# Optimization experiments

Hardware: AMD Instinct MI355X
Metric: run time of the kernel (lower is better)

Reference implementation:

```python
import jax, jax.numpy as jnp
import numpy as np

NUM_HEADS = 8
D_MODEL = 512
HEAD_DIM = D_MODEL // NUM_HEADS
LN_EPS = 1e-5


def setup_inputs() -> dict:
    key = jax.random.key(0)
    ks = jax.random.split(key, 12)
    B, S = 8, 1024
    P = 2 * S - 1  # relative position length
    s = 0.02
    return {
        "x": jax.random.normal(ks[0], (B, S, D_MODEL), jnp.float32),
        "pos_emb": jax.random.normal(ks[1], (P, D_MODEL), jnp.float32),
        "ln_w": jnp.ones((D_MODEL,), jnp.float32),
        "ln_b": jnp.zeros((D_MODEL,), jnp.float32),
        "Wq": jax.random.normal(ks[2], (D_MODEL, D_MODEL), jnp.float32) * s,
        "bq": jax.random.normal(ks[3], (D_MODEL,), jnp.float32) * s,
        "Wk": jax.random.normal(ks[4], (D_MODEL, D_MODEL), jnp.float32) * s,
        "bk": jax.random.normal(ks[5], (D_MODEL,), jnp.float32) * s,
        "Wv": jax.random.normal(ks[6], (D_MODEL, D_MODEL), jnp.float32) * s,
        "bv": jax.random.normal(ks[7], (D_MODEL,), jnp.float32) * s,
        "Wo": jax.random.normal(ks[8], (D_MODEL, D_MODEL), jnp.float32) * s,
        "bo": jax.random.normal(ks[9], (D_MODEL,), jnp.float32) * s,
        "Wp": jax.random.normal(ks[10], (D_MODEL, D_MODEL), jnp.float32) * s,
        "pos_bias_u": jax.random.normal(ks[11], (D_MODEL,), jnp.float32) * s,
        "pos_bias_v": jax.random.normal(jax.random.fold_in(key, 99), (D_MODEL,), jnp.float32) * s,
    }


def _rel_shift(x):
    # x: [B, H, S, P] -> Transformer-XL relative shift, return [B, H, S, S]
    b, h, s, p = x.shape
    x = jnp.pad(x, ((0, 0), (0, 0), (0, 0), (1, 0)))  # pad one zero column on left
    x = x.reshape(b, h, p + 1, s)[:, :, 1:, :]
    x = x.reshape(b, h, s, p)
    return x[:, :, :, :s]


def reference(x, pos_emb, ln_w, ln_b, Wq, bq, Wk, bk, Wv, bv, Wo, bo, Wp,
              pos_bias_u, pos_bias_v):
    B, S, D = x.shape
    H, hd = NUM_HEADS, HEAD_DIM
    # LayerNorm
    mu = jnp.mean(x, axis=-1, keepdims=True)
    var = jnp.mean(jnp.square(x - mu), axis=-1, keepdims=True)
    h_ = (x - mu) * jax.lax.rsqrt(var + LN_EPS) * ln_w + ln_b
    # Projections (torch Linear: y = x @ W.T + b)
    q = (h_ @ Wq.T + bq).reshape(B, S, H, hd).transpose(0, 2, 1, 3)  # [B,H,S,hd]
    k = (h_ @ Wk.T + bk).reshape(B, S, H, hd).transpose(0, 2, 1, 3)
    v = (h_ @ Wv.T + bv).reshape(B, S, H, hd).transpose(0, 2, 1, 3)
    bias_u = pos_bias_u.reshape(1, H, 1, hd)
    bias_v = pos_bias_v.reshape(1, H, 1, hd)
    content = jnp.einsum('bhqd,bhkd->bhqk', q + bias_u, k)
    # Positional projection: [P, D] -> [H, P, hd]
    p = (pos_emb @ Wp.T).reshape(-1, H, hd).transpose(1, 0, 2)
    pos_score = jnp.einsum('bhqd,hpd->bhqp', q + bias_v, p)
    pos_score = _rel_shift(pos_score)
    scale = 1.0 / np.sqrt(hd).astype(np.float32)
    attn = jax.nn.softmax((content + pos_score) * scale, axis=-1)
    out = jnp.einsum('bhqk,bhkd->bhqd', attn, v)
    out = out.transpose(0, 2, 1, 3).reshape(B, S, D)
    out = out @ Wo.T + bo
    return x + out
```

## Files before the change

kernel.cpp:

```cpp
#include <hip/hip_runtime.h>
#include <hip/hip_bf16.h>


typedef __attribute__((ext_vector_type(8))) short  s16x8;
typedef __attribute__((ext_vector_type(8))) __bf16 bfv8;
typedef __attribute__((ext_vector_type(4))) float  f32x4;
typedef __attribute__((ext_vector_type(4))) unsigned u32x4;

__device__ __forceinline__ float b2f(short s){
  unsigned u = ((unsigned)(unsigned short)s) << 16;
  float f; __builtin_memcpy(&f, &u, 4); return f;
}
__device__ __forceinline__ short f2b(float f){
  unsigned u; __builtin_memcpy(&u, &f, 4);
  u = (u + 0x7fffu + ((u >> 16) & 1u)) >> 16;
  return (short)u;
}
__device__ __forceinline__ unsigned pk2(float lo, float hi){
  __hip_bfloat162 t = __float22bfloat162_rn(make_float2(lo, hi));
  unsigned u; __builtin_memcpy(&u, &t, 4); return u;
}
__device__ __forceinline__ f32x4 MFMA(s16x8 a, s16x8 b, f32x4 c){
  return __builtin_amdgcn_mfma_f32_16x16x32_bf16(
      __builtin_bit_cast(bfv8, a), __builtin_bit_cast(bfv8, b), c, 0, 0, 0);
}
__device__ __forceinline__ void gload_lds16(const void* g, void* l){
  __builtin_amdgcn_global_load_lds(
      (const __attribute__((address_space(1))) void*)g,
      (__attribute__((address_space(3))) void*)l, 16, 0, 0);
}
__device__ __forceinline__ void cvt8(const float* in, short* out, size_t i8){
  f32x4 a = *(const f32x4*)(in + i8*8);
  f32x4 b = *(const f32x4*)(in + i8*8 + 4);
  u32x4 o;
  o[0] = pk2(a[0],a[1]); o[1] = pk2(a[2],a[3]);
  o[2] = pk2(b[0],b[1]); o[3] = pk2(b[2],b[3]);
  *(u32x4*)(out + i8*8) = o;
}

__global__ __launch_bounds__(256) void prep_kernel(
    const float* __restrict__ Wq, const float* __restrict__ Wk,
    const float* __restrict__ Wv, const float* __restrict__ Wo,
    const float* __restrict__ Wp, const float* __restrict__ pos,
    const float* __restrict__ x, const float* __restrict__ lnw, const float* __restrict__ lnb,
    short* __restrict__ wqkv, short* __restrict__ wo, short* __restrict__ wp,
    short* __restrict__ posbf, short* __restrict__ h_bf)
{
  int bid = blockIdx.x, tid = threadIdx.x;
  if(bid < 640){
    int w = bid >> 7;
    size_t i = (size_t)(bid & 127)*256 + tid;
    const float* src; short* dst;
    if(w == 0){ src = Wq; dst = wqkv; }
    else if(w == 1){ src = Wk; dst = wqkv + 262144; }
    else if(w == 2){ src = Wv; dst = wqkv + 524288; }
    else if(w == 3){ src = Wo; dst = wo; }
    else { src = Wp; dst = wp; }
    cvt8(src, dst, i);
  } else if(bid < 1152){
    size_t i = (size_t)(bid - 640)*256 + tid;
    if(i < 131008) cvt8(pos, posbf, i);
  } else {
    int row = (bid - 1152)*4 + (tid >> 6);
    int lane = tid & 63;
    const float* xr = x + (size_t)row*512;
    f32x4 v0 = *(const f32x4*)(xr + lane*8);
    f32x4 v1 = *(const f32x4*)(xr + lane*8 + 4);
    float s  = v0[0]+v0[1]+v0[2]+v0[3]+v1[0]+v1[1]+v1[2]+v1[3];
    float s2 = v0[0]*v0[0]+v0[1]*v0[1]+v0[2]*v0[2]+v0[3]*v0[3]
             + v1[0]*v1[0]+v1[1]*v1[1]+v1[2]*v1[2]+v1[3]*v1[3];
    #pragma unroll
    for(int m=1;m<64;m<<=1){ s += __shfl_xor(s,m); s2 += __shfl_xor(s2,m); }
    float mu = s * (1.0f/512.0f);
    float rs = rsqrtf(s2*(1.0f/512.0f) - mu*mu + 1e-5f);
    float y[8];
    #pragma unroll
    for(int e=0;e<8;e++){
      float xv = (e<4)? v0[e] : v1[e-4];
      int d = lane*8 + e;
      y[e] = (xv - mu)*rs*lnw[d] + lnb[d];
    }
    u32x4 o;
    o[0]=pk2(y[0],y[1]); o[1]=pk2(y[2],y[3]); o[2]=pk2(y[4],y[5]); o[3]=pk2(y[6],y[7]);
    *(u32x4*)(h_bf + (size_t)row*512 + lane*8) = o;
  }
}

__global__ __launch_bounds__(256) void gemm_fused(
    const short* __restrict__ h_bf, const short* __restrict__ wqkv,
    const float* __restrict__ bq, const float* __restrict__ bk, const float* __restrict__ bv,
    const short* __restrict__ posbf, const short* __restrict__ wp,
    short* __restrict__ q_sw, short* __restrict__ k_sw, short* __restrict__ v_sw,
    short* __restrict__ p_sw)
{
  __shared__ __align__(16) short smem[9216];
  short* At = smem;
  short* Bt = smem + 4096;
  int bid = blockIdx.x, tid = threadIdx.x;
  int wave = tid >> 6, lane = tid & 63;
  int quad = lane >> 4, l16 = lane & 15;
  int srow = lane >> 2, scol = (lane & 3)*8;
  if(bid < 768){
    int bx = bid % 12, by = bid / 12;
    int m0 = by*128, n0 = bx*128;
    int wm = wave >> 1, wn = wave & 1;
    f32x4 acc[4][4] = {};
    for(int k0=0; k0<512; k0+=32){
      #pragma unroll
      for(int c=0;c<2;c++){
        int rb = (wave + 4*c)*16;
        gload_lds16(h_bf + (size_t)(m0 + rb + srow)*512 + k0 + scol, At + rb*32);
        gload_lds16(wqkv + (size_t)(n0 + rb + srow)*512 + k0 + scol, Bt + rb*32);
      }
      __syncthreads();
      s16x8 af[4], bfr[4];
      #pragma unroll
      for(int i=0;i<4;i++) af[i]  = *(const s16x8*)(At + (wm*64 + i*16 + l16)*32 + quad*8);
      #pragma unroll
      for(int j=0;j<4;j++) bfr[j] = *(const s16x8*)(Bt + (wn*64 + j*16 + l16)*32 + quad*8);
      #pragma unroll
      for(int i=0;i<4;i++)
        #pragma unroll
        for(int j=0;j<4;j++)
          acc[i][j] = MFMA(af[i], bfr[j], acc[i][j]);
      __syncthreads();
    }
    int seg = bx >> 2;
    int nseg = (bx & 3)*128;
    int bb = by >> 3;
    const float* bsrc = (seg==0)? bq : (seg==1)? bk : bv;
    float bias_j[4];
    #pragma unroll
    for(int j=0;j<4;j++) bias_j[j] = bsrc[nseg + wn*64 + j*16 + l16];
    if(seg < 2){
      short* dst = seg ? k_sw : q_sw;
      #pragma unroll
      for(int h2=0; h2<2; h2++){
        if(wm == h2){
          #pragma unroll
          for(int i=0;i<4;i++){
            int lr = i*16 + quad*4;
            #pragma unroll
            for(int j=0;j<4;j++){
              int cl = wn*64 + j*16 + l16;
              unsigned p01 = pk2(acc[i][j][0]+bias_j[j], acc[i][j][1]+bias_j[j]);
              unsigned p23 = pk2(acc[i][j][2]+bias_j[j], acc[i][j][3]+bias_j[j]);
              smem[(lr+0)*136 + cl] = (short)p01;
              smem[(lr+1)*136 + cl] = (short)(p01>>16);
              smem[(lr+2)*136 + cl] = (short)p23;
              smem[(lr+3)*136 + cl] = (short)(p23>>16);
            }
          }
        }
        __syncthreads();
        #pragma unroll
        for(int it=0; it<4; it++){
          int ci = it*4 + wave;
          int hs = ci >> 2, tb = ci & 3;
          s16x8 vv = *(const s16x8*)(smem + (tb*16 + l16)*136 + hs*32 + quad*8);
          int hh = (nseg>>6) + (hs>>1);
          int tg = ((m0 + h2*64)>>4) + tb;
          size_t chunk = ((size_t)((bb*8 + hh)*64 + tg))*2 + (hs&1);
          *(s16x8*)(dst + chunk*512 + (size_t)lane*8) = vv;
        }
        __syncthreads();
      }
    } else {
      #pragma unroll
      for(int h2=0; h2<2; h2++){
        int jt = by*2 + h2;
        if(wm == h2){
          #pragma unroll
          for(int i=0;i<4;i++){
            int tl = i*16 + quad*4;
            #pragma unroll
            for(int j=0;j<4;j++){
              int dl = wn*64 + j*16 + l16;
              unsigned p01 = pk2(acc[i][j][0]+bias_j[j], acc[i][j][1]+bias_j[j]);
              unsigned p23 = pk2(acc[i][j][2]+bias_j[j], acc[i][j][3]+bias_j[j]);
              unsigned* w2 = (unsigned*)(smem + dl*72 + tl);
              w2[0] = p01; w2[1] = p23;
            }
          }
        }
        __syncthreads();
        #pragma unroll
        for(int it=0; it<4; it++){
          int ci = it*4 + wave;
          int hl = ci>>3, ds = (ci>>1)&3, jk = ci&1;
          s16x8 vv = *(const s16x8*)(smem + (hl*64 + ds*16 + l16)*72 + jk*32 + quad*8);
          int hh = (nseg>>6) + hl;
          size_t chunk = (((size_t)((bb*8 + hh)*16 + jt))*4 + ds)*2 + jk;
          *(s16x8*)(v_sw + chunk*512 + (size_t)lane*8) = vv;
        }
        __syncthreads();
      }
    }
  } else {
    int pid = bid - 768;
    int bx = pid % 8, by = pid / 8;
    int m0 = by*64, n0 = bx*64;
    int wm = wave >> 1, wn = wave & 1;
    f32x4 acc[2][2] = {};
    for(int k0=0; k0<512; k0+=32){
      int rb = wave*16;
      int ra = m0 + rb + srow; if(ra > 2046) ra = 2046;
      gload_lds16(posbf + (size_t)ra*512 + k0 + scol, At + rb*32);
      gload_lds16(wp + (size_t)(n0 + rb + srow)*512 + k0 + scol, Bt + rb*32);
      __syncthreads();
      s16x8 af[2], bfr[2];
      #pragma unroll
      for(int i=0;i<2;i++) af[i]  = *(const s16x8*)(At + (wm*32 + i*16 + l16)*32 + quad*8);
      #pragma unroll
      for(int j=0;j<2;j++) bfr[j] = *(const s16x8*)(Bt + (wn*32 + j*16 + l16)*32 + quad*8);
      #pragma unroll
      for(int i=0;i<2;i++)
        #pragma unroll
        for(int j=0;j<2;j++)
          acc[i][j] = MFMA(af[i], bfr[j], acc[i][j]);
      __syncthreads();
    }
    #pragma unroll
    for(int i=0;i<2;i++){
      int rowb = m0 + wm*32 + i*16 + quad*4;
      #pragma unroll
      for(int j=0;j<2;j++){
        int col = n0 + wn*32 + j*16 + l16;
        int hh = col>>6, ks = (col>>5)&1, qd = (col>>3)&3, e = col&7;
        int rblk = rowb>>4;
        size_t base = ((size_t)(((hh*128+rblk)*2+ks)*64) + qd*16)*8 + e;
        #pragma unroll
        for(int r=0;r<4;r++)
          p_sw[base + (size_t)(quad*4+r)*8] = f2b(acc[i][j][r]);
      }
    }
  }
}

__global__ __launch_bounds__(256) void attn_kernel(
    const short* __restrict__ q_sw, const short* __restrict__ k_sw,
    const short* __restrict__ v_sw, const short* __restrict__ p_sw,
    const float* __restrict__ bu, const float* __restrict__ bvv,
    short* __restrict__ out)
{
  __shared__ __align__(16) float combf[4160];
  int tid = threadIdx.x;
  int wave = tid >> 6, lane = tid & 63, quad = lane >> 4, l16 = lane & 15;
  int h = blockIdx.y, b = blockIdx.z, bh = b*8 + h;
  int iblk = blockIdx.x;
  int iw = iblk*16;
  short* pw = (short*)combf + wave*1152;

  const short* qb = q_sw + (size_t)bh*65536;
  const short* kb = k_sw + (size_t)bh*65536;
  const short* vb = v_sw + (size_t)bh*65536;
  const short* pb = p_sw + (size_t)h*131072;

  s16x8 qu[2], qv[2];
  #pragma unroll
  for(int ks=0;ks<2;ks++){
    s16x8 qr = *(const s16x8*)(qb + ((size_t)(iblk*2+ks)*64 + lane)*8);
    short tu[8], tv[8];
    #pragma unroll
    for(int e=0;e<8;e++){
      int d = h*64 + ks*32 + quad*8 + e;
      float f = b2f(qr[e]);
      tu[e] = f2b((f + bu[d]) * 0.125f);
      tv[e] = f2b((f + bvv[d]) * 0.125f);
    }
    qu[ks] = *(s16x8*)tu; qv[ks] = *(s16x8*)tv;
  }

  s16x8 ones;
  #pragma unroll
  for(int e=0;e<8;e++) ones[e] = (short)0x3F80;

  int srcl[4]; bool lo[4];
  #pragma unroll
  for(int r=0;r<4;r++){
    int il = quad*4 + r;
    srcl[r] = quad*16 + ((l16 + 15 - il) & 15);
    lo[r]   = (l16 <= il);
  }

  f32x4 oacc[4] = {};
  f32x4 lacc = {};

  #pragma unroll
  for(int t=0; t<4; t++){
    int jt = wave*4 + t;
    int rb0 = (jt*64 - iw + 1008) >> 4;
    f32x4 ps[5];
    #pragma unroll
    for(int nt=0;nt<5;nt++){
      f32x4 a = {};
      #pragma unroll
      for(int ks=0;ks<2;ks++){
        s16x8 pf = *(const s16x8*)(pb + ((size_t)((rb0+nt)*2+ks)*64 + lane)*8);
        a = MFMA(qv[ks], pf, a);
      }
      ps[nt] = a;
    }
    float rot[4][5];
    #pragma unroll
    for(int r=0;r<4;r++)
      #pragma unroll
      for(int nt=0;nt<5;nt++) rot[r][nt] = __shfl(ps[nt][r], srcl[r]);
    float pe[4][4];
    #pragma unroll
    for(int js=0;js<4;js++){
      f32x4 c0;
      #pragma unroll
      for(int r=0;r<4;r++) c0[r] = lo[r] ? rot[r][js] : rot[r][js+1];
      f32x4 a = c0;
      #pragma unroll
      for(int ks=0;ks<2;ks++){
        s16x8 kf = *(const s16x8*)(kb + ((size_t)((jt*4+js)*2+ks)*64 + lane)*8);
        a = MFMA(qu[ks], kf, a);
      }
      #pragma unroll
      for(int r=0;r<4;r++) pe[js][r] = __expf(a[r]);
    }
    #pragma unroll
    for(int js=0;js<4;js++){
      int col = js*16 + l16;
      unsigned p01 = pk2(pe[js][0], pe[js][1]);
      unsigned p23 = pk2(pe[js][2], pe[js][3]);
      pw[(quad*4+0)*72 + col] = (short)p01;
      pw[(quad*4+1)*72 + col] = (short)(p01>>16);
      pw[(quad*4+2)*72 + col] = (short)p23;
      pw[(quad*4+3)*72 + col] = (short)(p23>>16);
    }
    #pragma unroll
    for(int jk=0;jk<2;jk++){
      s16x8 pf = *(const s16x8*)(pw + l16*72 + jk*32 + quad*8);
      #pragma unroll
      for(int ds=0;ds<4;ds++){
        s16x8 vf = *(const s16x8*)(vb + ((size_t)((jt*4+ds)*2+jk)*64 + lane)*8);
        oacc[ds] = MFMA(pf, vf, oacc[ds]);
      }
      lacc = MFMA(pf, ones, lacc);
    }
  }
  __syncthreads();
  float* comb  = combf;
  float* lcomb = combf + 4096;
  #pragma unroll
  for(int e=0;e<16;e++) comb[wave*1024 + e*64 + lane] = oacc[e>>2][e&3];
  if(l16 == 0){
    #pragma unroll
    for(int r=0;r<4;r++) lcomb[wave*16 + quad*4 + r] = lacc[r];
  }
  __syncthreads();
  #pragma unroll
  for(int i=0;i<4;i++){
    int s = i*256 + tid;
    int e = s >> 6, lsrc = s & 63;
    int ds = e >> 2, rr = e & 3;
    int il = (lsrc >> 4)*4 + rr;
    int dim = ds*16 + (lsrc & 15);
    float o = comb[s] + comb[1024+s] + comb[2048+s] + comb[3072+s];
    float l = lcomb[il] + lcomb[16+il] + lcomb[32+il] + lcomb[48+il];
    float rl = __builtin_amdgcn_rcpf(l);
    out[((size_t)(b*1024 + iw + il)*512) + h*64 + dim] = f2b(o * rl);
  }
}

__global__ __launch_bounds__(256) void gemm_out(
    const short* __restrict__ A, const short* __restrict__ B,
    const float* __restrict__ bias, const float* __restrict__ resid,
    float* __restrict__ Cout)
{
  __shared__ __align__(16) short At[64*32];
  __shared__ __align__(16) short Bt[64*32];
  int tid = threadIdx.x;
  int wave = tid >> 6, lane = tid & 63;
  int quad = lane >> 4, l16 = lane & 15;
  int wm = wave >> 1, wn = wave & 1;
  int m0 = blockIdx.y*64, n0 = blockIdx.x*64;
  int srow = lane >> 2, scol = (lane & 3)*8;
  f32x4 acc[2][2] = {};
  for(int k0=0; k0<512; k0+=32){
    int rb = wave*16;
    gload_lds16(A + (size_t)(m0 + rb + srow)*512 + k0 + scol, At + rb*32);
    gload_lds16(B + (size_t)(n0 + rb + srow)*512 + k0 + scol, Bt + rb*32);
    __syncthreads();
    s16x8 af[2], bfr[2];
    #pragma unroll
    for(int i=0;i<2;i++) af[i]  = *(const s16x8*)(At + (wm*32 + i*16 + l16)*32 + quad*8);
    #pragma unroll
    for(int j=0;j<2;j++) bfr[j] = *(const s16x8*)(Bt + (wn*32 + j*16 + l16)*32 + quad*8);
    #pragma unroll
    for(int i=0;i<2;i++)
      #pragma unroll
      for(int j=0;j<2;j++)
        acc[i][j] = MFMA(af[i], bfr[j], acc[i][j]);
    __syncthreads();
  }
  #pragma unroll
  for(int i=0;i<2;i++){
    int rowb = m0 + wm*32 + i*16 + quad*4;
    #pragma unroll
    for(int j=0;j<2;j++){
      int col = n0 + wn*32 + j*16 + l16;
      float bv = bias[col];
      #pragma unroll
      for(int r=0;r<4;r++){
        size_t idx = (size_t)(rowb + r)*512 + col;
        Cout[idx] = acc[i][j][r] + bv + resid[idx];
      }
    }
  }
}

extern "C" void kernel_launch(void* const* d_in, const int* in_sizes, int n_in,
                              void* d_out, int out_size, void* d_ws, size_t ws_size,
                              hipStream_t stream)
{
  const float* x    = (const float*)d_in[0];
  const float* pos  = (const float*)d_in[1];
  const float* lnw  = (const float*)d_in[2];
  const float* lnb  = (const float*)d_in[3];
  const float* Wq   = (const float*)d_in[4];
  const float* bq   = (const float*)d_in[5];
  const float* Wk   = (const float*)d_in[6];
  const float* bk   = (const float*)d_in[7];
  const float* Wv   = (const float*)d_in[8];
  const float* bv   = (const float*)d_in[9];
  const float* Wo   = (const float*)d_in[10];
  const float* bo   = (const float*)d_in[11];
  const float* Wp   = (const float*)d_in[12];
  const float* pbu  = (const float*)d_in[13];
  const float* pbv  = (const float*)d_in[14];
  float* out = (float*)d_out;

  char* ws = (char*)d_ws;
  short* h_bf    = (short*)(ws);
  short* q_sw    = (short*)(ws + ( 8u<<20));
  short* k_sw    = (short*)(ws + (16u<<20));
  short* v_sw    = (short*)(ws + (24u<<20));
  short* a_bf    = (short*)(ws + (32u<<20));
  short* p_sw    = (short*)(ws + (40u<<20));
  short* pos_bf  = (short*)(ws + (42u<<20));
  short* wqkv_bf = (short*)(ws + (44u<<20));
  short* wo_bf   = (short*)(ws + (47u<<20));
  short* wp_bf   = (short*)(ws + (47u<<20) + (512u<<10));

  prep_kernel<<<dim3(3200), 256, 0, stream>>>(Wq, Wk, Wv, Wo, Wp, pos,
                                              x, lnw, lnb,
                                              wqkv_bf, wo_bf, wp_bf, pos_bf, h_bf);
  gemm_fused<<<dim3(1024), 256, 0, stream>>>(h_bf, wqkv_bf, bq, bk, bv,
                                             pos_bf, wp_bf,
                                             q_sw, k_sw, v_sw, p_sw);
  attn_kernel<<<dim3(64,8,8), 256, 0, stream>>>(q_sw, k_sw, v_sw, p_sw, pbu, pbv, a_bf);
  gemm_out<<<dim3(8,128), 256, 0, stream>>>(a_bf, wo_bf, bo, x, out);
  (void)in_sizes; (void)n_in; (void)out_size; (void)ws_size;
}
```

Before: 211.0 us.

## Process two query sub-blocks per attention block to reuse K, V and P fragments

Each attention workgroup now handles 32 query rows (two 16-row sub-blocks) instead of 16, so every K, V and positional fragment loaded from global memory feeds two sets of MFMAs. The positional tiles are shared across the two sub-blocks through a 6-tile sliding window, since the second sub-block's relative-position window is offset by one tile. The grid is halved, shared memory doubled, launch bounds set to 3 blocks per CU, and s_setprio hints wrap the MFMA phases. The cost is more registers per thread and fewer workgroups, which could reduce occupancy and latency hiding.

```diff
diff --git a/kernel.cpp b/kernel.cpp
--- a/kernel.cpp
+++ b/kernel.cpp
@@ -237,38 +237,41 @@
   }
 }
 
-__global__ __launch_bounds__(256) void attn_kernel(
+__global__ __launch_bounds__(256, 3) void attn_kernel(
     const short* __restrict__ q_sw, const short* __restrict__ k_sw,
     const short* __restrict__ v_sw, const short* __restrict__ p_sw,
     const float* __restrict__ bu, const float* __restrict__ bvv,
     short* __restrict__ out)
 {
-  __shared__ __align__(16) float combf[4160];
+  __shared__ __align__(16) float combf[8320];
   int tid = threadIdx.x;
   int wave = tid >> 6, lane = tid & 63, quad = lane >> 4, l16 = lane & 15;
   int h = blockIdx.y, b = blockIdx.z, bh = b*8 + h;
-  int iblk = blockIdx.x;
-  int iw = iblk*16;
-  short* pw = (short*)combf + wave*1152;
+  int qblk = blockIdx.x;
+  int iw = qblk*32;
+  short* pw = (short*)combf + wave*2304;
 
   const short* qb = q_sw + (size_t)bh*65536;
   const short* kb = k_sw + (size_t)bh*65536;
   const short* vb = v_sw + (size_t)bh*65536;
   const short* pb = p_sw + (size_t)h*131072;
 
-  s16x8 qu[2], qv[2];
-  #pragma unroll
-  for(int ks=0;ks<2;ks++){
-    s16x8 qr = *(const s16x8*)(qb + ((size_t)(iblk*2+ks)*64 + lane)*8);
-    short tu[8], tv[8];
-    #pragma unroll
-    for(int e=0;e<8;e++){
-      int d = h*64 + ks*32 + quad*8 + e;
-      float f = b2f(qr[e]);
-      tu[e] = f2b((f + bu[d]) * 0.125f);
-      tv[e] = f2b((f + bvv[d]) * 0.125f);
-    }
-    qu[ks] = *(s16x8*)tu; qv[ks] = *(s16x8*)tv;
+  s16x8 qu[2][2], qv[2][2];
+  #pragma unroll
+  for(int s=0;s<2;s++){
+    #pragma unroll
+    for(int ks=0;ks<2;ks++){
+      s16x8 qr = *(const s16x8*)(qb + ((size_t)((qblk*2+s)*2+ks)*64 + lane)*8);
+      short tu[8], tv[8];
+      #pragma unroll
+      for(int e=0;e<8;e++){
+        int d = h*64 + ks*32 + quad*8 + e;
+        float f = b2f(qr[e]);
+        tu[e] = f2b((f + bu[d]) * 0.125f);
+        tv[e] = f2b((f + bvv[d]) * 0.125f);
+      }
+      qu[s][ks] = *(s16x8*)tu; qv[s][ks] = *(s16x8*)tv;
+    }
   }
 
   s16x8 ones;
@@ -283,86 +286,117 @@
     lo[r]   = (l16 <= il);
   }
 
-  f32x4 oacc[4] = {};
-  f32x4 lacc = {};
+  f32x4 oacc[2][4] = {};
+  f32x4 lacc[2] = {};
 
   #pragma unroll
   for(int t=0; t<4; t++){
     int jt = wave*4 + t;
     int rb0 = (jt*64 - iw + 1008) >> 4;
-    f32x4 ps[5];
-    #pragma unroll
-    for(int nt=0;nt<5;nt++){
-      f32x4 a = {};
-      #pragma unroll
-      for(int ks=0;ks<2;ks++){
-        s16x8 pf = *(const s16x8*)(pb + ((size_t)((rb0+nt)*2+ks)*64 + lane)*8);
-        a = MFMA(qv[ks], pf, a);
-      }
-      ps[nt] = a;
-    }
-    float rot[4][5];
-    #pragma unroll
-    for(int r=0;r<4;r++)
-      #pragma unroll
-      for(int nt=0;nt<5;nt++) rot[r][nt] = __shfl(ps[nt][r], srcl[r]);
-    float pe[4][4];
+    f32x4 ps0[5], ps1[5];
+    __builtin_amdgcn_s_setprio(1);
+    #pragma unroll
+    for(int nt=0;nt<6;nt++){
+      int rbp = rb0 - 1 + nt;
+      s16x8 pf0 = *(const s16x8*)(pb + ((size_t)(rbp*2+0)*64 + lane)*8);
+      s16x8 pf1 = *(const s16x8*)(pb + ((size_t)(rbp*2+1)*64 + lane)*8);
+      if(nt >= 1){
+        f32x4 a = {};
+        a = MFMA(qv[0][0], pf0, a);
+        a = MFMA(qv[0][1], pf1, a);
+        ps0[nt-1] = a;
+      }
+      if(nt <= 4){
+        f32x4 a = {};
+        a = MFMA(qv[1][0], pf0, a);
+        a = MFMA(qv[1][1], pf1, a);
+        ps1[nt] = a;
+      }
+    }
+    __builtin_amdgcn_s_setprio(0);
+    float rot0[4][5], rot1[4][5];
+    #pragma unroll
+    for(int r=0;r<4;r++){
+      #pragma unroll
+      for(int nt=0;nt<5;nt++){
+        rot0[r][nt] = __shfl(ps0[nt][r], srcl[r]);
+        rot1[r][nt] = __shfl(ps1[nt][r], srcl[r]);
+      }
+    }
     #pragma unroll
     for(int js=0;js<4;js++){
-      f32x4 c0;
-      #pragma unroll
-      for(int r=0;r<4;r++) c0[r] = lo[r] ? rot[r][js] : rot[r][js+1];
-      f32x4 a = c0;
-      #pragma unroll
-      for(int ks=0;ks<2;ks++){
-        s16x8 kf = *(const s16x8*)(kb + ((size_t)((jt*4+js)*2+ks)*64 + lane)*8);
-        a = MFMA(qu[ks], kf, a);
-      }
-      #pragma unroll
-      for(int r=0;r<4;r++) pe[js][r] = __expf(a[r]);
-    }
-    #pragma unroll
-    for(int js=0;js<4;js++){
+      s16x8 kf0 = *(const s16x8*)(kb + ((size_t)((jt*4+js)*2+0)*64 + lane)*8);
+      s16x8 kf1 = *(const s16x8*)(kb + ((size_t)((jt*4+js)*2+1)*64 + lane)*8);
       int col = js*16 + l16;
-      unsigned p01 = pk2(pe[js][0], pe[js][1]);
-      unsigned p23 = pk2(pe[js][2], pe[js][3]);
-      pw[(quad*4+0)*72 + col] = (short)p01;
-      pw[(quad*4+1)*72 + col] = (short)(p01>>16);
-      pw[(quad*4+2)*72 + col] = (short)p23;
-      pw[(quad*4+3)*72 + col] = (short)(p23>>16);
-    }
+      {
+        f32x4 c0;
+        #pragma unroll
+        for(int r=0;r<4;r++) c0[r] = lo[r] ? rot0[r][js] : rot0[r][js+1];
+        f32x4 a = MFMA(qu[0][0], kf0, c0);
+        a = MFMA(qu[0][1], kf1, a);
+        unsigned p01 = pk2(__expf(a[0]), __expf(a[1]));
+        unsigned p23 = pk2(__expf(a[2]), __expf(a[3]));
+        pw[(quad*4+0)*72 + col] = (short)p01;
+        pw[(quad*4+1)*72 + col] = (short)(p01>>16);
+        pw[(quad*4+2)*72 + col] = (short)p23;
+        pw[(quad*4+3)*72 + col] = (short)(p23>>16);
+      }
+      {
+        f32x4 c0;
+        #pragma unroll
+        for(int r=0;r<4;r++) c0[r] = lo[r] ? rot1[r][js] : rot1[r][js+1];
+        f32x4 a = MFMA(qu[1][0], kf0, c0);
+        a = MFMA(qu[1][1], kf1, a);
+        unsigned p01 = pk2(__expf(a[0]), __expf(a[1]));
+        unsigned p23 = pk2(__expf(a[2]), __expf(a[3]));
+        pw[1152 + (quad*4+0)*72 + col] = (short)p01;
+        pw[1152 + (quad*4+1)*72 + col] = (short)(p01>>16);
+        pw[1152 + (quad*4+2)*72 + col] = (short)p23;
+        pw[1152 + (quad*4+3)*72 + col] = (short)(p23>>16);
+      }
+    }
+    __builtin_amdgcn_s_setprio(1);
     #pragma unroll
     for(int jk=0;jk<2;jk++){
-      s16x8 pf = *(const s16x8*)(pw + l16*72 + jk*32 + quad*8);
+      s16x8 pa0 = *(const s16x8*)(pw + l16*72 + jk*32 + quad*8);
+      s16x8 pa1 = *(const s16x8*)(pw + 1152 + l16*72 + jk*32 + quad*8);
+      lacc[0] = MFMA(pa0, ones, lacc[0]);
+      lacc[1] = MFMA(pa1, ones, lacc[1]);
       #pragma unroll
       for(int ds=0;ds<4;ds++){
         s16x8 vf = *(const s16x8*)(vb + ((size_t)((jt*4+ds)*2+jk)*64 + lane)*8);
-        oacc[ds] = MFMA(pf, vf, oacc[ds]);
-      }
-      lacc = MFMA(pf, ones, lacc);
-    }
+        oacc[0][ds] = MFMA(pa0, vf, oacc[0][ds]);
+        oacc[1][ds] = MFMA(pa1, vf, oacc[1][ds]);
+      }
+    }
+    __builtin_amdgcn_s_setprio(0);
   }
   __syncthreads();
   float* comb  = combf;
-  float* lcomb = combf + 4096;
-  #pragma unroll
-  for(int e=0;e<16;e++) comb[wave*1024 + e*64 + lane] = oacc[e>>2][e&3];
-  if(l16 == 0){
-    #pragma unroll
-    for(int r=0;r<4;r++) lcomb[wave*16 + quad*4 + r] = lacc[r];
+  float* lcomb = combf + 8192;
+  #pragma unroll
+  for(int s=0;s<2;s++){
+    #pragma unroll
+    for(int e=0;e<16;e++) comb[wave*2048 + s*1024 + e*64 + lane] = oacc[s][e>>2][e&3];
+    if(l16 == 0){
+      #pragma unroll
+      for(int r=0;r<4;r++) lcomb[wave*32 + s*16 + quad*4 + r] = lacc[s][r];
+    }
   }
   __syncthreads();
   #pragma unroll
-  for(int i=0;i<4;i++){
-    int s = i*256 + tid;
-    int e = s >> 6, lsrc = s & 63;
+  for(int i=0;i<8;i++){
+    int v = i*256 + tid;
+    int lsrc = v & 63;
+    int e = (v >> 6) & 15;
+    int s = v >> 10;
     int ds = e >> 2, rr = e & 3;
     int il = (lsrc >> 4)*4 + rr;
     int dim = ds*16 + (lsrc & 15);
-    float o = comb[s] + comb[1024+s] + comb[2048+s] + comb[3072+s];
-    float l = lcomb[il] + lcomb[16+il] + lcomb[32+il] + lcomb[48+il];
+    float o = comb[v] + comb[2048+v] + comb[4096+v] + comb[6144+v];
+    float l = lcomb[s*16+il] + lcomb[32+s*16+il] + lcomb[64+s*16+il] + lcomb[96+s*16+il];
     float rl = __builtin_amdgcn_rcpf(l);
-    out[((size_t)(b*1024 + iw + il)*512) + h*64 + dim] = f2b(o * rl);
+    out[((size_t)(b*1024 + iw + s*16 + il)*512) + h*64 + dim] = f2b(o * rl);
   }
 }
 
@@ -452,7 +486,7 @@
   gemm_fused<<<dim3(1024), 256, 0, stream>>>(h_bf, wqkv_bf, bq, bk, bv,
                                              pos_bf, wp_bf,
                                              q_sw, k_sw, v_sw, p_sw);
-  attn_kernel<<<dim3(64,8,8), 256, 0, stream>>>(q_sw, k_sw, v_sw, p_sw, pbu, pbv, a_bf);
+  attn_kernel<<<dim3(32,8,8), 256, 0, stream>>>(q_sw, k_sw, v_sw, p_sw, pbu, pbv, a_bf);
   gemm_out<<<dim3(8,128), 256, 0, stream>>>(a_bf, wo_bf, bo, x, out);
   (void)in_sizes; (void)n_in; (void)out_size; (void)ws_size;
 }
```

New measurement: 202.2 us. -4.2%, faster.

## Restructure attention so each wave owns query rows and K/V tiles are shared via LDS

Applied to the files above, without the earlier changes.

Changes the attention split: each wave now handles its own 16 query rows across all key tiles, instead of four waves splitting keys for one row block and reducing at the end. K/V tiles are staged into double-buffered LDS with direct global-to-LDS loads and shared by the four waves. Positional fragments are prefetched into registers one tile ahead, and the MFMA sections run at raised wave priority. This removes the cross-wave reduction and cuts repeated global K/V loads, at the cost of more LDS, a sync per tile and a 4x smaller grid.

```diff
diff --git a/kernel.cpp b/kernel.cpp
--- a/kernel.cpp
+++ b/kernel.cpp
@@ -237,19 +237,20 @@
   }
 }
 
-__global__ __launch_bounds__(256) void attn_kernel(
+__global__ __launch_bounds__(256, 3) void attn_kernel(
     const short* __restrict__ q_sw, const short* __restrict__ k_sw,
     const short* __restrict__ v_sw, const short* __restrict__ p_sw,
     const float* __restrict__ bu, const float* __restrict__ bvv,
     short* __restrict__ out)
 {
-  __shared__ __align__(16) float combf[4160];
+  __shared__ __align__(16) short kv[2][8192];
+  __shared__ __align__(16) short pwall[4608];
   int tid = threadIdx.x;
   int wave = tid >> 6, lane = tid & 63, quad = lane >> 4, l16 = lane & 15;
   int h = blockIdx.y, b = blockIdx.z, bh = b*8 + h;
-  int iblk = blockIdx.x;
+  int iblk = blockIdx.x*4 + wave;
   int iw = iblk*16;
-  short* pw = (short*)combf + wave*1152;
+  short* pw = pwall + wave*1152;
 
   const short* qb = q_sw + (size_t)bh*65536;
   const short* kb = k_sw + (size_t)bh*65536;
@@ -285,85 +286,97 @@
 
   f32x4 oacc[4] = {};
   f32x4 lacc = {};
-
-  #pragma unroll
-  for(int t=0; t<4; t++){
-    int jt = wave*4 + t;
+  s16x8 Pa[5][2];
+
+  auto STAGE = [&](int jt, int bufi){
+    const short* base = (wave < 2) ? kb : vb;
+    #pragma unroll
+    for(int r=0;r<4;r++){
+      int unit = wave*4 + r;
+      gload_lds16(base + (size_t)jt*4096 + (unit&7)*512 + lane*8,
+                  &kv[bufi][unit*512]);
+    }
+  };
+  auto LOADPOS = [&](int jt){
     int rb0 = (jt*64 - iw + 1008) >> 4;
+    #pragma unroll
+    for(int nt=0;nt<5;nt++)
+      #pragma unroll
+      for(int ks=0;ks<2;ks++)
+        Pa[nt][ks] = *(const s16x8*)(pb + (size_t)((rb0+nt)*2+ks)*512 + lane*8);
+  };
+  auto COMPUTE = [&](const short* Kt, const short* Vt, int next_jt){
     f32x4 ps[5];
+    __builtin_amdgcn_s_setprio(1);
     #pragma unroll
     for(int nt=0;nt<5;nt++){
       f32x4 a = {};
-      #pragma unroll
-      for(int ks=0;ks<2;ks++){
-        s16x8 pf = *(const s16x8*)(pb + ((size_t)((rb0+nt)*2+ks)*64 + lane)*8);
-        a = MFMA(qv[ks], pf, a);
-      }
+      a = MFMA(qv[0], Pa[nt][0], a);
+      a = MFMA(qv[1], Pa[nt][1], a);
       ps[nt] = a;
     }
+    __builtin_amdgcn_s_setprio(0);
+    if(next_jt < 16) LOADPOS(next_jt);
     float rot[4][5];
     #pragma unroll
     for(int r=0;r<4;r++)
       #pragma unroll
       for(int nt=0;nt<5;nt++) rot[r][nt] = __shfl(ps[nt][r], srcl[r]);
-    float pe[4][4];
     #pragma unroll
     for(int js=0;js<4;js++){
+      s16x8 kf0 = *(const s16x8*)(Kt + (js*2+0)*512 + lane*8);
+      s16x8 kf1 = *(const s16x8*)(Kt + (js*2+1)*512 + lane*8);
       f32x4 c0;
       #pragma unroll
       for(int r=0;r<4;r++) c0[r] = lo[r] ? rot[r][js] : rot[r][js+1];
-      f32x4 a = c0;
-      #pragma unroll
-      for(int ks=0;ks<2;ks++){
-        s16x8 kf = *(const s16x8*)(kb + ((size_t)((jt*4+js)*2+ks)*64 + lane)*8);
-        a = MFMA(qu[ks], kf, a);
-      }
-      #pragma unroll
-      for(int r=0;r<4;r++) pe[js][r] = __expf(a[r]);
-    }
-    #pragma unroll
-    for(int js=0;js<4;js++){
+      f32x4 a = MFMA(qu[0], kf0, c0);
+      a = MFMA(qu[1], kf1, a);
       int col = js*16 + l16;
-      unsigned p01 = pk2(pe[js][0], pe[js][1]);
-      unsigned p23 = pk2(pe[js][2], pe[js][3]);
+      unsigned p01 = pk2(__expf(a[0]), __expf(a[1]));
+      unsigned p23 = pk2(__expf(a[2]), __expf(a[3]));
       pw[(quad*4+0)*72 + col] = (short)p01;
       pw[(quad*4+1)*72 + col] = (short)(p01>>16);
       pw[(quad*4+2)*72 + col] = (short)p23;
       pw[(quad*4+3)*72 + col] = (short)(p23>>16);
     }
+    __builtin_amdgcn_s_setprio(1);
     #pragma unroll
     for(int jk=0;jk<2;jk++){
-      s16x8 pf = *(const s16x8*)(pw + l16*72 + jk*32 + quad*8);
+      s16x8 pa = *(const s16x8*)(pw + l16*72 + jk*32 + quad*8);
+      lacc = MFMA(pa, ones, lacc);
       #pragma unroll
       for(int ds=0;ds<4;ds++){
-        s16x8 vf = *(const s16x8*)(vb + ((size_t)((jt*4+ds)*2+jk)*64 + lane)*8);
-        oacc[ds] = MFMA(pf, vf, oacc[ds]);
-      }
-      lacc = MFMA(pf, ones, lacc);
-    }
-  }
+        s16x8 vf = *(const s16x8*)(Vt + (ds*2+jk)*512 + lane*8);
+        oacc[ds] = MFMA(pa, vf, oacc[ds]);
+      }
+    }
+    __builtin_amdgcn_s_setprio(0);
+  };
+
+  STAGE(0, 0);
+  LOADPOS(0);
   __syncthreads();
-  float* comb  = combf;
-  float* lcomb = combf + 4096;
-  #pragma unroll
-  for(int e=0;e<16;e++) comb[wave*1024 + e*64 + lane] = oacc[e>>2][e&3];
-  if(l16 == 0){
-    #pragma unroll
-    for(int r=0;r<4;r++) lcomb[wave*16 + quad*4 + r] = lacc[r];
-  }
-  __syncthreads();
-  #pragma unroll
-  for(int i=0;i<4;i++){
-    int s = i*256 + tid;
-    int e = s >> 6, lsrc = s & 63;
-    int ds = e >> 2, rr = e & 3;
-    int il = (lsrc >> 4)*4 + rr;
-    int dim = ds*16 + (lsrc & 15);
-    float o = comb[s] + comb[1024+s] + comb[2048+s] + comb[3072+s];
-    float l = lcomb[il] + lcomb[16+il] + lcomb[32+il] + lcomb[48+il];
-    float rl = __builtin_amdgcn_rcpf(l);
-    out[((size_t)(b*1024 + iw + il)*512) + h*64 + dim] = f2b(o * rl);
-  }
+
+  #pragma unroll 1
+  for(int jt2=0; jt2<8; ++jt2){
+    int jt = jt2*2;
+    STAGE(jt+1, 1);
+    COMPUTE(&kv[0][0], &kv[0][4096], jt+1);
+    __syncthreads();
+    if(jt2 < 7) STAGE(jt+2, 0);
+    COMPUTE(&kv[1][0], &kv[1][4096], jt+2);
+    __syncthreads();
+  }
+
+  float rl[4];
+  #pragma unroll
+  for(int r=0;r<4;r++) rl[r] = __builtin_amdgcn_rcpf(lacc[r]);
+  #pragma unroll
+  for(int ds=0; ds<4; ds++)
+    #pragma unroll
+    for(int r=0;r<4;r++)
+      out[((size_t)(b*1024 + iw + quad*4 + r))*512 + h*64 + ds*16 + l16] =
+          f2b(oacc[ds][r] * rl[r]);
 }
 
 __global__ __launch_bounds__(256) void gemm_out(
@@ -452,7 +465,7 @@
   gemm_fused<<<dim3(1024), 256, 0, stream>>>(h_bf, wqkv_bf, bq, bk, bv,
                                              pos_bf, wp_bf,
                                              q_sw, k_sw, v_sw, p_sw);
-  attn_kernel<<<dim3(64,8,8), 256, 0, stream>>>(q_sw, k_sw, v_sw, p_sw, pbu, pbv, a_bf);
+  attn_kernel<<<dim3(16,8,8), 256, 0, stream>>>(q_sw, k_sw, v_sw, p_sw, pbu, pbv, a_bf);
   gemm_out<<<dim3(8,128), 256, 0, stream>>>(a_bf, wo_bf, bo, x, out);
   (void)in_sizes; (void)n_in; (void)out_size; (void)ws_size;
 }
```

Result: faster. 199.0 us (-5.7%).
